# Performance work log

Hardware: AMD Instinct MI355X
Metric: run time of the kernel (lower is better)

The kernel has to match this reference:

```python
import jax, jax.numpy as jnp
import numpy as np

B, M, K, KNN = 2, 256, 64, 16
CXYZ, CFEAT = 3, 61
CIN = CXYZ + CFEAT  # 64
MLPS = [64, 128]
SUMM = sum(MLPS)    # 192
CALIB = 64
EXP = [256, 512]
OUT = 256
EPS = 1e-5


def bn(x, g, b):
    # BatchNorm eval mode with running_mean=0, running_var=1 (channel axis 1)
    shape = (1, -1) + (1,) * (x.ndim - 2)
    return x * (g / jnp.sqrt(1.0 + EPS)).reshape(shape) + b.reshape(shape)


def knn(x, k):
    xx = jnp.sum(x * x, axis=1)                      # (B, N)
    inner = jnp.einsum('bcn,bcm->bnm', x, x)         # (B, N, N)
    pd = 2.0 * inner - xx[:, :, None] - xx[:, None, :]
    return jax.lax.top_k(pd, k)[1]                   # (B, N, k)


def graph_feature(x, idx):
    # x: (B, C, N), idx: (B, N, k) -> (B, 2C, N, k)
    xt = jnp.transpose(x, (0, 2, 1))                 # (B, N, C)
    nb = jax.vmap(lambda a, i: a[i])(xt, idx)        # (B, N, k, C)
    ctr = xt[:, :, None, :]
    feat = jnp.concatenate([nb - ctr, jnp.broadcast_to(ctr, nb.shape)], axis=-1)
    return jnp.transpose(feat, (0, 3, 1, 2))


def forward(xyz, feats, e1_w, e1_g, e1_b, e2_w, e2_g, e2_b,
            cal1_w, cal1_g, cal1_b, cal2_w, cal2_bias,
            exp1_w, exp1_g, exp1_b, exp2_w, exp2_g, exp2_b,
            red_w, red_g, red_b, sc1_w, sc1_b, sc2_w, sc2_b,
            sc_n1_g, sc_n1_b, sc_n2_g, sc_n2_b):
    x3 = xyz.reshape(B * M, K, CXYZ).transpose(0, 2, 1)      # (BM, 3, K)
    f = feats.reshape(B * M, K, CFEAT).transpose(0, 2, 1)    # (BM, 61, K)
    idx = knn(x3, KNN)                                        # USE_FEATS_DIS=False: knn once on xyz
    x = jnp.concatenate([x3, f], axis=1)                      # (BM, 64, K)
    outs = []
    for W, g, b in ((e1_w, e1_g, e1_b), (e2_w, e2_g, e2_b)):
        gf = graph_feature(x, idx)                            # (BM, 2C, K, knn)
        y = jax.nn.relu(bn(jnp.einsum('oc,bcnk->bonk', W, gf), g, b))
        x = y.max(axis=-1)                                    # (BM, mlp_i, K)
        outs.append(x)
    x = jnp.concatenate(outs, axis=1)                         # (BM, 192, K)
    c = jax.nn.relu(bn(jnp.einsum('oc,bcn->bon', cal1_w, x), cal1_g, cal1_b))
    c = jnp.einsum('oc,bcn->bon', cal2_w, c) + cal2_bias[None, :, None]
    x = jax.nn.sigmoid(c) * x
    x = jax.nn.relu(bn(jnp.einsum('oc,bcn->bon', exp1_w, x), exp1_g, exp1_b))
    x = jax.nn.relu(bn(jnp.einsum('oc,bcn->bon', exp2_w, x), exp2_g, exp2_b))
    x = x.max(axis=-1).reshape(B, M, EXP[1]).transpose(0, 2, 1)  # (B, 512, M)
    x = jax.nn.relu(bn(jnp.einsum('oc,bcm->bom', red_w, x), red_g, red_b))
    x = bn(x + x, sc_n1_g, sc_n1_b)
    h = jax.nn.relu(jnp.einsum('oc,bcm->bom', sc1_w, x) + sc1_b[None, :, None])
    h = jnp.einsum('oc,bcm->bom', sc2_w, h) + sc2_b[None, :, None]
    x = bn(x + h, sc_n2_g, sc_n2_b)
    return x                                                  # (B, 256, M)


def setup_inputs() -> dict:
    key = jax.random.key(0)
    ks = jax.random.split(key, 16)
    w = lambda k, s: jax.random.normal(k, s, jnp.float32) * 0.05
    ones = lambda n: jnp.ones((n,), jnp.float32)
    zeros = lambda n: jnp.zeros((n,), jnp.float32)
    return {
        'xyz': jax.random.normal(ks[0], (B, M, K, CXYZ), jnp.float32),
        'feats': jax.random.normal(ks[1], (B, M, K, CFEAT), jnp.float32),
        'e1_w': w(ks[2], (MLPS[0], 2 * CIN)), 'e1_g': ones(MLPS[0]), 'e1_b': zeros(MLPS[0]),
        'e2_w': w(ks[3], (MLPS[1], 2 * MLPS[0])), 'e2_g': ones(MLPS[1]), 'e2_b': zeros(MLPS[1]),
        'cal1_w': w(ks[4], (CALIB, SUMM)), 'cal1_g': ones(CALIB), 'cal1_b': zeros(CALIB),
        'cal2_w': w(ks[5], (SUMM, CALIB)), 'cal2_bias': zeros(SUMM),
        'exp1_w': w(ks[6], (EXP[0], SUMM)), 'exp1_g': ones(EXP[0]), 'exp1_b': zeros(EXP[0]),
        'exp2_w': w(ks[7], (EXP[1], EXP[0])), 'exp2_g': ones(EXP[1]), 'exp2_b': zeros(EXP[1]),
        'red_w': w(ks[8], (OUT, EXP[1])), 'red_g': ones(OUT), 'red_b': zeros(OUT),
        'sc1_w': w(ks[9], (OUT, OUT)), 'sc1_b': zeros(OUT),
        'sc2_w': w(ks[10], (OUT, OUT)), 'sc2_b': zeros(OUT),
        'sc_n1_g': ones(OUT), 'sc_n1_b': zeros(OUT),
        'sc_n2_g': ones(OUT), 'sc_n2_b': zeros(OUT),
    }


def reference(xyz, feats, e1_w, e1_g, e1_b, e2_w, e2_g, e2_b,
              cal1_w, cal1_g, cal1_b, cal2_w, cal2_bias,
              exp1_w, exp1_g, exp1_b, exp2_w, exp2_g, exp2_b,
              red_w, red_g, red_b, sc1_w, sc1_b, sc2_w, sc2_b,
              sc_n1_g, sc_n1_b, sc_n2_g, sc_n2_b):
    return forward(xyz, feats, e1_w, e1_g, e1_b, e2_w, e2_g, e2_b,
                   cal1_w, cal1_g, cal1_b, cal2_w, cal2_bias,
                   exp1_w, exp1_g, exp1_b, exp2_w, exp2_g, exp2_b,
                   red_w, red_g, red_b, sc1_w, sc1_b, sc2_w, sc2_b,
                   sc_n1_g, sc_n1_b, sc_n2_g, sc_n2_b)
```

## Files before the change

### kernel.cpp

```cpp
#include <hip/hip_runtime.h>
#include <hip/hip_bf16.h>
#include <math.h>
#include <stddef.h>

#define DEV __device__ __forceinline__
__device__ const float BNS = 0.99999500003749968f;

typedef __bf16 bf16x8 __attribute__((ext_vector_type(8)));
typedef float  f32x4  __attribute__((ext_vector_type(4)));

DEV unsigned short f2bs(float v){
  union{ __hip_bfloat16 b; unsigned short u; } c; c.b=__float2bfloat16(v); return c.u;
}
DEV float bs2f(unsigned short u){
  union{ unsigned short u; __hip_bfloat16 b; } c; c.u=u; return __bfloat162float(c.b);
}


__global__ __launch_bounds__(256) void k_prep(const float* __restrict__ e1_w,
    const float* __restrict__ e2_w, const float* __restrict__ cal1_w,
    const float* __restrict__ cal2_w, const float* __restrict__ exp1_w,
    const float* __restrict__ exp2_w, unsigned short* __restrict__ Whi,
    unsigned short* __restrict__ Wlo,
    const float* __restrict__ red_w, const float* __restrict__ sc1_w,
    const float* __restrict__ sc2_w, float* __restrict__ Wt_red,
    float* __restrict__ Wt_s1, float* __restrict__ Wt_s2){
  __shared__ float s[32][33];
  int bid = blockIdx.x;
  if(bid < 896){
    const float* src; unsigned short *hi,*lo; int mode, O=0, i0;
    if(bid<32)      { src=e1_w;  hi=Whi;       lo=Wlo;       mode=1; O= 64; i0=bid*256; }
    else if(bid<96) { src=e2_w;  hi=Whi+8192;  lo=Wlo+8192;  mode=1; O=128; i0=(bid-32)*256; }
    else if(bid<144){ src=cal1_w;hi=Whi+24576; lo=Wlo+24576; mode=0;        i0=(bid-96)*256; }
    else if(bid<192){ src=cal2_w;hi=Whi+36864; lo=Wlo+36864; mode=0;        i0=(bid-144)*256; }
    else if(bid<384){ src=exp1_w;hi=Whi+49152; lo=Wlo+49152; mode=0;        i0=(bid-192)*256; }
    else            { src=exp2_w;hi=Whi+98304; lo=Wlo+98304; mode=0;        i0=(bid-384)*256; }
    int i = i0 + threadIdx.x;
    float v;
    if(mode==0) v = src[i];
    else {
      int row=i>>6, c=i&63;
      v = (row<O) ? src[row*128+c] : (src[(row-O)*128+64+c]-src[(row-O)*128+c]);
    }
    unsigned short h=f2bs(v); hi[i]=h; lo[i]=f2bs(v-bs2f(h));
  } else {
    int lb = bid-896;
    const float* in; float* out; int O,K;
    if(lb<128){ in=red_w; out=Wt_red; O=256; K=512; }
    else if(lb<192){ in=sc1_w; out=Wt_s1; O=256; K=256; lb-=128; }
    else { in=sc2_w; out=Wt_s2; O=256; K=256; lb-=192; }
    int nt=O>>5;
    int to=lb%nt, tk=lb/nt;
    int c=threadIdx.x&31, r8=threadIdx.x>>5;
    #pragma unroll
    for(int p=0;p<4;p++){
      int r=r8+p*8;
      s[r][c]=in[(size_t)(to*32+r)*K + tk*32 + c];
    }
    __syncthreads();
    #pragma unroll
    for(int p=0;p<4;p++){
      int r=r8+p*8;
      out[(size_t)(tk*32+r)*O + to*32 + c]=s[c][r];
    }
  }
}

__global__ __launch_bounds__(256) void k_knne12(const float* __restrict__ xyz,
    const float* __restrict__ feats,
    const unsigned short* __restrict__ W1h, const unsigned short* __restrict__ W1l,
    const unsigned short* __restrict__ W2h, const unsigned short* __restrict__ W2l,
    int* __restrict__ idxo, const float* __restrict__ g1, const float* __restrict__ b1,
    const float* __restrict__ g2, const float* __restrict__ b2,
    unsigned short* __restrict__ cat){
  __shared__ float bufA[64*65];
  __shared__ float bufB[64*65];
  __shared__ __align__(16) unsigned short sb[64*136];
  __shared__ int   ips[64*16];
  __shared__ float sx0[64], sx1[64], sx2[64], sxx[64];
  int bm = blockIdx.x;
  int tid = threadIdx.x, n = tid&63, s = tid>>6;
  int wid = tid>>6, lane = tid&63;
  int l15 = lane&15, q = lane>>4;
  if(s==0){
    const float* xp = xyz + (size_t)(bm*64+n)*3;
    float px=xp[0], py=xp[1], pz=xp[2];
    sx0[n]=px; sx1[n]=py; sx2[n]=pz; sxx[n]=px*px+py*py+pz*pz;
  }
  __syncthreads();
  {
    int p = lane>>2, seg = lane&3;
    int n1 = wid*16 + p;
    float px=sx0[n1], py=sx1[n1], pz=sx2[n1], xxn=sxx[n1];
    float pdr[16];
    #pragma unroll
    for(int t=0;t<16;t++){
      int m = seg*16+t;
      pdr[t] = 2.f*(px*sx0[m]+py*sx1[m]+pz*sx2[m]) - xxn - sxx[m];
    }
    for(int j=0;j<16;j++){
      float bv=-3.4e38f; int bi=seg*16;
      #pragma unroll
      for(int t=0;t<16;t++){ if(pdr[t]>bv){bv=pdr[t]; bi=seg*16+t;} }
      float ov=__shfl_xor(bv,1); int oi=__shfl_xor(bi,1);
      if(ov>bv || (ov==bv && oi<bi)){bv=ov;bi=oi;}
      ov=__shfl_xor(bv,2); oi=__shfl_xor(bi,2);
      if(ov>bv || (ov==bv && oi<bi)){bv=ov;bi=oi;}
      if(seg==0) ips[n1*16+j]=bi;
      if((bi>>4)==seg) pdr[bi&15]=-3.4e38f;
    }
  }
  {
    unsigned short* r = sb + n*136;
    if(s==0){
      float px=sx0[n], py=sx1[n], pz=sx2[n];
      unsigned short h;
      h=f2bs(px); r[0]=h; r[64]=f2bs(px-bs2f(h));
      h=f2bs(py); r[1]=h; r[65]=f2bs(py-bs2f(h));
      h=f2bs(pz); r[2]=h; r[66]=f2bs(pz-bs2f(h));
    }
    const float* fp = feats + (size_t)(bm*64+n)*61;
    #pragma unroll
    for(int t=0;t<16;t++){
      int cc = s*16+t;
      if(cc<61){
        float v=fp[cc]; unsigned short h=f2bs(v);
        r[3+cc]=h; r[64+3+cc]=f2bs(v-bs2f(h));
      }
    }
  }
  __syncthreads();
  #pragma unroll
  for(int t=0;t<4;t++) idxo[bm*1024 + tid*4 + t] = ips[tid*4 + t];
  {
    int rbase = ((wid<2)?0:64) + (wid&1)*32;
    f32x4 acc[2][4];
    #pragma unroll
    for(int a=0;a<2;a++)
      #pragma unroll
      for(int d=0;d<4;d++) acc[a][d]=(f32x4){0.f,0.f,0.f,0.f};
    #pragma unroll
    for(int kc=0;kc<2;kc++){
      int k0=kc*32;
      size_t a0=(size_t)(rbase+l15)*64 + k0 + q*8;
      size_t a1=(size_t)(rbase+16+l15)*64 + k0 + q*8;
      bf16x8 a0h=*(const bf16x8*)(W1h+a0), a0l=*(const bf16x8*)(W1l+a0);
      bf16x8 a1h=*(const bf16x8*)(W1h+a1), a1l=*(const bf16x8*)(W1l+a1);
      #pragma unroll
      for(int nt=0;nt<4;nt++){
        int row = nt*16 + l15;
        bf16x8 bh = *(const bf16x8*)&sb[row*136 + k0 + q*8];
        bf16x8 bl = *(const bf16x8*)&sb[row*136 + 64 + k0 + q*8];
        acc[0][nt]=__builtin_amdgcn_mfma_f32_16x16x32_bf16(a0h,bh,acc[0][nt],0,0,0);
        acc[0][nt]=__builtin_amdgcn_mfma_f32_16x16x32_bf16(a0h,bl,acc[0][nt],0,0,0);
        acc[0][nt]=__builtin_amdgcn_mfma_f32_16x16x32_bf16(a0l,bh,acc[0][nt],0,0,0);
        acc[1][nt]=__builtin_amdgcn_mfma_f32_16x16x32_bf16(a1h,bh,acc[1][nt],0,0,0);
        acc[1][nt]=__builtin_amdgcn_mfma_f32_16x16x32_bf16(a1h,bl,acc[1][nt],0,0,0);
        acc[1][nt]=__builtin_amdgcn_mfma_f32_16x16x32_bf16(a1l,bh,acc[1][nt],0,0,0);
      }
    }
    __syncthreads();
    float* dst = (wid<2)? bufA : bufB;
    int ro = (wid&1)*32;
    #pragma unroll
    for(int mt=0;mt<2;mt++)
      #pragma unroll
      for(int nt=0;nt<4;nt++)
        #pragma unroll
        for(int rr=0;rr<4;rr++)
          dst[(ro+mt*16+q*4+rr)*65 + nt*16+l15] = acc[mt][nt][rr];
  }
  __syncthreads();
  {
    int o = lane;
    float sc = g1[o]*BNS, bi = b1[o];
    #pragma unroll 4
    for(int j=0;j<16;j++){
      int nn = wid*16 + j;
      const int* ip = &ips[nn*16];
      float mz = -3.4e38f;
      #pragma unroll
      for(int k=0;k<16;k++) mz = fmaxf(mz, bufA[o*65 + ip[k]]);
      float v = fmaxf(sc*(mz + bufB[o*65 + nn]) + bi, 0.f);
      unsigned short hv = f2bs(v), lv = f2bs(v - bs2f(hv));
      size_t cb = ((size_t)bm*64+nn)*384 + o;
      cat[cb] = hv; cat[cb+192] = lv;
      sb[nn*136 + o] = hv; sb[nn*136 + 64 + o] = lv;
    }
  }
  for(int ch=0; ch<2; ch++){
    __syncthreads();
    int rbase = ((wid<2)?0:128) + ch*64 + (wid&1)*32;
    f32x4 acc[2][4];
    #pragma unroll
    for(int a=0;a<2;a++)
      #pragma unroll
      for(int d=0;d<4;d++) acc[a][d]=(f32x4){0.f,0.f,0.f,0.f};
    #pragma unroll
    for(int kc=0;kc<2;kc++){
      int k0=kc*32;
      size_t a0=(size_t)(rbase+l15)*64 + k0 + q*8;
      size_t a1=(size_t)(rbase+16+l15)*64 + k0 + q*8;
      bf16x8 a0h=*(const bf16x8*)(W2h+a0), a0l=*(const bf16x8*)(W2l+a0);
      bf16x8 a1h=*(const bf16x8*)(W2h+a1), a1l=*(const bf16x8*)(W2l+a1);
      #pragma unroll
      for(int nt=0;nt<4;nt++){
        int row = nt*16 + l15;
        bf16x8 bh = *(const bf16x8*)&sb[row*136 + k0 + q*8];
        bf16x8 bl = *(const bf16x8*)&sb[row*136 + 64 + k0 + q*8];
        acc[0][nt]=__builtin_amdgcn_mfma_f32_16x16x32_bf16(a0h,bh,acc[0][nt],0,0,0);
        acc[0][nt]=__builtin_amdgcn_mfma_f32_16x16x32_bf16(a0h,bl,acc[0][nt],0,0,0);
        acc[0][nt]=__builtin_amdgcn_mfma_f32_16x16x32_bf16(a0l,bh,acc[0][nt],0,0,0);
        acc[1][nt]=__builtin_amdgcn_mfma_f32_16x16x32_bf16(a1h,bh,acc[1][nt],0,0,0);
        acc[1][nt]=__builtin_amdgcn_mfma_f32_16x16x32_bf16(a1h,bl,acc[1][nt],0,0,0);
        acc[1][nt]=__builtin_amdgcn_mfma_f32_16x16x32_bf16(a1l,bh,acc[1][nt],0,0,0);
      }
    }
    __syncthreads();
    float* dst = (wid<2)? bufA : bufB;
    int ro = (wid&1)*32;
    #pragma unroll
    for(int mt=0;mt<2;mt++)
      #pragma unroll
      for(int nt=0;nt<4;nt++)
        #pragma unroll
        for(int rr=0;rr<4;rr++)
          dst[(ro+mt*16+q*4+rr)*65 + nt*16+l15] = acc[mt][nt][rr];
    __syncthreads();
    int o = ch*64 + lane;
    float sc = g2[o]*BNS, bi = b2[o];
    #pragma unroll 4
    for(int j=0;j<16;j++){
      int nn = wid*16 + j;
      const int* ip = &ips[nn*16];
      float mz = -3.4e38f;
      #pragma unroll
      for(int k=0;k<16;k++) mz = fmaxf(mz, bufA[lane*65 + ip[k]]);
      float v = fmaxf(sc*(mz + bufB[lane*65 + nn]) + bi, 0.f);
      unsigned short hv = f2bs(v);
      size_t cb = ((size_t)bm*64+nn)*384 + 64 + o;
      cat[cb] = hv; cat[cb+192] = f2bs(v - bs2f(hv));
    }
  }
}

__global__ __launch_bounds__(256) void k_cal(
    const unsigned short* __restrict__ Whi, const unsigned short* __restrict__ Wlo,
    unsigned short* __restrict__ cats,
    const float* __restrict__ c1g, const float* __restrict__ c1b,
    const float* __restrict__ c2bias){
  const unsigned short* c1w_h = Whi+24576; const unsigned short* c1w_l = Wlo+24576;
  const unsigned short* c2w_h = Whi+36864; const unsigned short* c2w_l = Wlo+36864;
  __shared__ __align__(16) unsigned short sW[64*64];
  __shared__ __align__(16) unsigned short sX[128*64];
  __shared__ __align__(16) unsigned short c1L[128*136];
  int rt = blockIdx.x;
  int tid = threadIdx.x, wid = tid>>6, lane = tid&63;
  int l15 = lane&15, q = lane>>4;
  f32x4 acc1[8];
  #pragma unroll
  for(int d=0;d<8;d++) acc1[d]=(f32x4){0.f,0.f,0.f,0.f};
  size_t xbase = (size_t)rt*128*384;
  for(int kc=0;kc<6;kc++){
    int k0=kc*32;
    __syncthreads();
    #pragma unroll
    for(int i=0;i<2;i++){
      int U = tid + i*256;
      int r = U>>3, up = U&7, u = up ^ (r&7);
      const unsigned short* src = (u<4)
        ? (c1w_h + (size_t)r*192 + k0 + u*8)
        : (c1w_l + (size_t)r*192 + k0 + (u-4)*8);
      *(uint4*)&sW[U*8] = *(const uint4*)src;
    }
    #pragma unroll
    for(int i=0;i<4;i++){
      int U = tid + i*256;
      int r = U>>3, up = U&7, u = up ^ (r&7);
      const unsigned short* src = cats + xbase + (size_t)r*384
        + (u<4 ? (size_t)(k0 + u*8) : (size_t)(192 + k0 + (u-4)*8));
      *(uint4*)&sX[U*8] = *(const uint4*)src;
    }
    __syncthreads();
    int o = wid*16 + l15;
    bf16x8 wh = *(const bf16x8*)&sW[(o*8 + ((  q) ^ (o&7)))*8];
    bf16x8 wl = *(const bf16x8*)&sW[(o*8 + ((4+q) ^ (o&7)))*8];
    #pragma unroll
    for(int nf=0;nf<8;nf++){
      int r = nf*16 + l15;
      bf16x8 xh = *(const bf16x8*)&sX[(r*8 + ((  q) ^ (r&7)))*8];
      bf16x8 xl = *(const bf16x8*)&sX[(r*8 + ((4+q) ^ (r&7)))*8];
      acc1[nf]=__builtin_amdgcn_mfma_f32_16x16x32_bf16(wh,xh,acc1[nf],0,0,0);
      acc1[nf]=__builtin_amdgcn_mfma_f32_16x16x32_bf16(wh,xl,acc1[nf],0,0,0);
      acc1[nf]=__builtin_amdgcn_mfma_f32_16x16x32_bf16(wl,xh,acc1[nf],0,0,0);
    }
  }
  {
    int ob0 = wid*16 + q*4;
    float s0[4], b0[4];
    #pragma unroll
    for(int r=0;r<4;r++){ s0[r]=c1g[ob0+r]*BNS; b0[r]=c1b[ob0+r]; }
    #pragma unroll
    for(int nf=0;nf<8;nf++){
      int n = nf*16 + l15;
      unsigned short hv[4], lv[4];
      #pragma unroll
      for(int r=0;r<4;r++){
        float v = fmaxf(acc1[nf][r]*s0[r]+b0[r], 0.f);
        hv[r]=f2bs(v); lv[r]=f2bs(v - bs2f(hv[r]));
      }
      *(ushort4*)&c1L[n*136 + ob0]      = make_ushort4(hv[0],hv[1],hv[2],hv[3]);
      *(ushort4*)&c1L[n*136 + 64 + ob0] = make_ushort4(lv[0],lv[1],lv[2],lv[3]);
    }
  }
  __syncthreads();
  f32x4 acc2[3][8];
  #pragma unroll
  for(int a=0;a<3;a++)
    #pragma unroll
    for(int d=0;d<8;d++) acc2[a][d]=(f32x4){0.f,0.f,0.f,0.f};
  #pragma unroll
  for(int kc=0;kc<2;kc++){
    int k0=kc*32;
    bf16x8 ah[3], al[3];
    #pragma unroll
    for(int mt=0;mt<3;mt++){
      int o = wid*48 + mt*16 + l15;
      ah[mt]=*(const bf16x8*)(c2w_h + (size_t)o*64 + k0 + q*8);
      al[mt]=*(const bf16x8*)(c2w_l + (size_t)o*64 + k0 + q*8);
    }
    #pragma unroll
    for(int nf=0;nf<8;nf++){
      int n = nf*16 + l15;
      bf16x8 bh = *(const bf16x8*)&c1L[n*136 + k0 + q*8];
      bf16x8 bl = *(const bf16x8*)&c1L[n*136 + 64 + k0 + q*8];
      #pragma unroll
      for(int mt=0;mt<3;mt++){
        acc2[mt][nf]=__builtin_amdgcn_mfma_f32_16x16x32_bf16(ah[mt],bh,acc2[mt][nf],0,0,0);
        acc2[mt][nf]=__builtin_amdgcn_mfma_f32_16x16x32_bf16(ah[mt],bl,acc2[mt][nf],0,0,0);
        acc2[mt][nf]=__builtin_amdgcn_mfma_f32_16x16x32_bf16(al[mt],bh,acc2[mt][nf],0,0,0);
      }
    }
  }
  #pragma unroll
  for(int mt=0;mt<3;mt++){
    int ob0 = wid*48 + mt*16 + q*4;
    float bi[4];
    #pragma unroll
    for(int r=0;r<4;r++) bi[r]=c2bias[ob0+r];
    #pragma unroll
    for(int nf=0;nf<8;nf++){
      size_t row = (size_t)rt*128 + nf*16 + l15;
      size_t rb = row*384;
      ushort4 hv = *(ushort4*)(cats + rb + ob0);
      ushort4 lv = *(ushort4*)(cats + rb + 192 + ob0);
      unsigned short h[4]={hv.x,hv.y,hv.z,hv.w}, l[4]={lv.x,lv.y,lv.z,lv.w};
      #pragma unroll
      for(int r=0;r<4;r++){
        float g = 1.f/(1.f+__expf(-(acc2[mt][nf][r]+bi[r])));
        float f = (bs2f(h[r])+bs2f(l[r]))*g;
        h[r]=f2bs(f); l[r]=f2bs(f-bs2f(h[r]));
      }
      *(ushort4*)(cats + rb + ob0)       = make_ushort4(h[0],h[1],h[2],h[3]);
      *(ushort4*)(cats + rb + 192 + ob0) = make_ushort4(l[0],l[1],l[2],l[3]);
    }
  }
}

template<int K, int BO, int EPI>
__global__ __launch_bounds__(256) void k_mm2(
    const unsigned short* __restrict__ Whi, const unsigned short* __restrict__ Wlo,
    const unsigned short* __restrict__ X, void* __restrict__ Og,
    const float* __restrict__ sg, const float* __restrict__ bg, int O){
  constexpr int WO = BO/4;
  constexpr int MT = WO/16;
  constexpr int WUNITS = BO*8;
  __shared__ __align__(16) unsigned short sW[BO*64];
  __shared__ __align__(16) unsigned short sX[128*64];
  int rt = blockIdx.x;
  int o0 = blockIdx.y*BO;
  int tid = threadIdx.x, wid = tid>>6, lane = tid&63;
  int l15 = lane&15, q = lane>>4;
  f32x4 acc[MT][8];
  #pragma unroll
  for(int a=0;a<MT;a++)
    #pragma unroll
    for(int d=0;d<8;d++) acc[a][d]=(f32x4){0.f,0.f,0.f,0.f};
  size_t xbase = (size_t)rt*128*2*K;
  for(int kc=0; kc<K/32; kc++){
    int k0 = kc*32;
    __syncthreads();
    #pragma unroll
    for(int i=0;i<WUNITS/256;i++){
      int U = tid + i*256;
      int r = U>>3, up = U&7, u = up ^ (r&7);
      const unsigned short* src = (u<4)
        ? (Whi + (size_t)(o0+r)*K + k0 + u*8)
        : (Wlo + (size_t)(o0+r)*K + k0 + (u-4)*8);
      *(uint4*)&sW[U*8] = *(const uint4*)src;
    }
    #pragma unroll
    for(int i=0;i<4;i++){
      int U = tid + i*256;
      int r = U>>3, up = U&7, u = up ^ (r&7);
      const unsigned short* src = X + xbase + (size_t)r*2*K
        + (u<4 ? (size_t)(k0 + u*8) : (size_t)(K + k0 + (u-4)*8));
      *(uint4*)&sX[U*8] = *(const uint4*)src;
    }
    __syncthreads();
    bf16x8 wf[MT][2];
    #pragma unroll
    for(int mt=0;mt<MT;mt++){
      int o = wid*WO + mt*16 + l15;
      wf[mt][0] = *(const bf16x8*)&sW[(o*8 + ((  q) ^ (o&7)))*8];
      wf[mt][1] = *(const bf16x8*)&sW[(o*8 + ((4+q) ^ (o&7)))*8];
    }
    #pragma unroll
    for(int nf=0;nf<8;nf++){
      int r = nf*16 + l15;
      bf16x8 xh = *(const bf16x8*)&sX[(r*8 + ((  q) ^ (r&7)))*8];
      bf16x8 xl = *(const bf16x8*)&sX[(r*8 + ((4+q) ^ (r&7)))*8];
      #pragma unroll
      for(int mt=0;mt<MT;mt++){
        acc[mt][nf]=__builtin_amdgcn_mfma_f32_16x16x32_bf16(wf[mt][0],xh,acc[mt][nf],0,0,0);
        acc[mt][nf]=__builtin_amdgcn_mfma_f32_16x16x32_bf16(wf[mt][0],xl,acc[mt][nf],0,0,0);
        acc[mt][nf]=__builtin_amdgcn_mfma_f32_16x16x32_bf16(wf[mt][1],xh,acc[mt][nf],0,0,0);
      }
    }
  }
  if(EPI==0){
    unsigned short* ob = (unsigned short*)Og;
    #pragma unroll
    for(int mt=0;mt<MT;mt++){
      int ob0 = o0 + wid*WO + mt*16 + q*4;
      float s0[4], b0[4];
      #pragma unroll
      for(int r=0;r<4;r++){ s0[r]=sg[ob0+r]*BNS; b0[r]=bg[ob0+r]; }
      #pragma unroll
      for(int nf=0;nf<8;nf++){
        size_t row = (size_t)rt*128 + nf*16 + l15;
        size_t rb = row*2*O;
        unsigned short hv[4], lv[4];
        #pragma unroll
        for(int r=0;r<4;r++){
          float v = fmaxf(acc[mt][nf][r]*s0[r]+b0[r], 0.f);
          hv[r]=f2bs(v); lv[r]=f2bs(v - bs2f(hv[r]));
        }
        *(ushort4*)(ob + rb + ob0)     = make_ushort4(hv[0],hv[1],hv[2],hv[3]);
        *(ushort4*)(ob + rb + O + ob0) = make_ushort4(lv[0],lv[1],lv[2],lv[3]);
      }
    }
  } else {
    float* pool = (float*)Og;
    #pragma unroll
    for(int mt=0;mt<MT;mt++){
      int ob0 = o0 + wid*WO + mt*16 + q*4;
      #pragma unroll
      for(int half=0;half<2;half++){
        int bm = 2*rt + half;
        int b = bm>>8, m = bm&255;
        #pragma unroll
        for(int r=0;r<4;r++){
          float s=sg[ob0+r]*BNS, bi=bg[ob0+r];
          float v = acc[mt][half*4+0][r]*s+bi;
          v = fmaxf(v, acc[mt][half*4+1][r]*s+bi);
          v = fmaxf(v, acc[mt][half*4+2][r]*s+bi);
          v = fmaxf(v, acc[mt][half*4+3][r]*s+bi);
          v = fmaxf(v, 0.f);
          v = fmaxf(v, __shfl_xor(v,1));
          v = fmaxf(v, __shfl_xor(v,2));
          v = fmaxf(v, __shfl_xor(v,4));
          v = fmaxf(v, __shfl_xor(v,8));
          if(l15==0) pool[((size_t)b*512 + ob0+r)*256 + m] = v;
        }
      }
    }
  }
}

__global__ __launch_bounds__(256) void k_headf(const float* __restrict__ Wt_red,
    const float* __restrict__ Wt_s1, const float* __restrict__ Wt_s2,
    const float* __restrict__ pool, float* __restrict__ Og,
    const float* __restrict__ red_g, const float* __restrict__ red_b,
    const float* __restrict__ n1g, const float* __restrict__ n1b,
    const float* __restrict__ s1b, const float* __restrict__ s2b,
    const float* __restrict__ n2g, const float* __restrict__ n2b){
  __shared__ float P[512*3];
  __shared__ float X1[256*3];
  __shared__ float H[256*3];
  int g = blockIdx.x;
  int b = g>>7, mg = g&127;
  int m0 = mg*2;
  int o = threadIdx.x;
  #pragma unroll
  for(int i=0;i<2;i++){
    int c = o + i*256;
    float2 v = *(const float2*)&pool[((size_t)b*512+c)*256 + m0];
    P[c*3+0]=v.x; P[c*3+1]=v.y;
  }
  __syncthreads();
  float a0,a1;
  a0=a1=0.f;
  #pragma unroll 8
  for(int c=0;c<512;c++){
    float w = Wt_red[c*256+o];
    a0 += w*P[c*3]; a1 += w*P[c*3+1];
  }
  float x0r,x1r;
  {
    float s=red_g[o]*BNS, bi=red_b[o], s1=n1g[o]*BNS, b1=n1b[o];
    float r0=fmaxf(a0*s+bi,0.f), r1=fmaxf(a1*s+bi,0.f);
    x0r=2.f*r0*s1+b1; x1r=2.f*r1*s1+b1;
    X1[o*3]=x0r; X1[o*3+1]=x1r;
  }
  __syncthreads();
  a0=a1=0.f;
  #pragma unroll 8
  for(int c=0;c<256;c++){
    float w = Wt_s1[c*256+o];
    a0 += w*X1[c*3]; a1 += w*X1[c*3+1];
  }
  {
    float bi=s1b[o];
    H[o*3]=fmaxf(a0+bi,0.f); H[o*3+1]=fmaxf(a1+bi,0.f);
  }
  __syncthreads();
  a0=a1=0.f;
  #pragma unroll 8
  for(int c=0;c<256;c++){
    float w = Wt_s2[c*256+o];
    a0 += w*H[c*3]; a1 += w*H[c*3+1];
  }
  {
    float bi=s2b[o], s2=n2g[o]*BNS, b2=n2b[o];
    float v0=(x0r+a0+bi)*s2+b2, v1=(x1r+a1+bi)*s2+b2;
    *(float2*)&Og[((size_t)b*256+o)*256 + m0] = make_float2(v0,v1);
  }
}

extern "C" void kernel_launch(void* const* d_in, const int* in_sizes, int n_in,
                              void* d_out, int out_size, void* d_ws, size_t ws_size,
                              hipStream_t stream){
  const float* xyz     =(const float*)d_in[0];
  const float* feats   =(const float*)d_in[1];
  const float* e1_w    =(const float*)d_in[2];
  const float* e1_g    =(const float*)d_in[3];
  const float* e1_b    =(const float*)d_in[4];
  const float* e2_w    =(const float*)d_in[5];
  const float* e2_g    =(const float*)d_in[6];
  const float* e2_b    =(const float*)d_in[7];
  const float* cal1_w  =(const float*)d_in[8];
  const float* cal1_g  =(const float*)d_in[9];
  const float* cal1_b  =(const float*)d_in[10];
  const float* cal2_w  =(const float*)d_in[11];
  const float* cal2_bias=(const float*)d_in[12];
  const float* exp1_w  =(const float*)d_in[13];
  const float* exp1_g  =(const float*)d_in[14];
  const float* exp1_b  =(const float*)d_in[15];
  const float* exp2_w  =(const float*)d_in[16];
  const float* exp2_g  =(const float*)d_in[17];
  const float* exp2_b  =(const float*)d_in[18];
  const float* red_w   =(const float*)d_in[19];
  const float* red_g   =(const float*)d_in[20];
  const float* red_b   =(const float*)d_in[21];
  const float* sc1_w   =(const float*)d_in[22];
  const float* sc1_b   =(const float*)d_in[23];
  const float* sc2_w   =(const float*)d_in[24];
  const float* sc2_b   =(const float*)d_in[25];
  const float* sc_n1_g =(const float*)d_in[26];
  const float* sc_n1_b =(const float*)d_in[27];
  const float* sc_n2_g =(const float*)d_in[28];
  const float* sc_n2_b =(const float*)d_in[29];

  char* wsb=(char*)d_ws;
  int*            idx =(int*)           (wsb);
  unsigned short* cats=(unsigned short*)(wsb + 10485760);
  unsigned short* p1s =(unsigned short*)(wsb + 35651584);
  float*          pool=(float*)         (wsb + 69206016);
  unsigned short* Whi =(unsigned short*)(wsb + 75497472);
  unsigned short* Wlo =(unsigned short*)(wsb + 76021760);
  float*          Wt_red=(float*)       (wsb + 76546048);
  float*          Wt_s1 =(float*)       (wsb + 77070336);
  float*          Wt_s2 =(float*)       (wsb + 77332480);
  unsigned short* e1e_h=Whi;          unsigned short* e1e_l=Wlo;
  unsigned short* e2e_h=Whi+8192;     unsigned short* e2e_l=Wlo+8192;
  unsigned short* e1w_h=Whi+49152;    unsigned short* e1w_l=Wlo+49152;
  unsigned short* e2w_h=Whi+98304;    unsigned short* e2w_l=Wlo+98304;

  k_prep      <<<1152,256,0,stream>>>(e1_w,e2_w,cal1_w,cal2_w,exp1_w,exp2_w,Whi,Wlo,
                                      red_w,sc1_w,sc2_w,Wt_red,Wt_s1,Wt_s2);
  k_knne12    <<<512,256,0,stream>>>(xyz,feats,e1e_h,e1e_l,e2e_h,e2e_l,idx,
                                     e1_g,e1_b,e2_g,e2_b,cats);
  k_cal       <<<256,256,0,stream>>>(Whi,Wlo,cats,cal1_g,cal1_b,cal2_bias);
  k_mm2<192,128,0><<<dim3(256,2),256,0,stream>>>(e1w_h,e1w_l,cats,(void*)p1s,exp1_g,exp1_b,256);
  k_mm2<256,128,2><<<dim3(256,4),256,0,stream>>>(e2w_h,e2w_l,p1s,(void*)pool,exp2_g,exp2_b,512);
  k_headf     <<<256,256,0,stream>>>(Wt_red,Wt_s1,Wt_s2,pool,(float*)d_out,
                                     red_g,red_b,sc_n1_g,sc_n1_b,sc1_b,sc2_b,sc_n2_g,sc_n2_b);
}
```

Measured before the change: 267.3 us.

## Fuse calibration and expansion MLPs into one per-group kernel, split head reduction

New measurement: 274.4 us. 1.03x slower.

```diff
diff --git a/kernel.cpp b/kernel.cpp
--- a/kernel.cpp
+++ b/kernel.cpp
@@ -9,11 +9,27 @@
 typedef __bf16 bf16x8 __attribute__((ext_vector_type(8)));
 typedef float  f32x4  __attribute__((ext_vector_type(4)));
 
+#define MF(a,b,c) __builtin_amdgcn_mfma_f32_16x16x32_bf16(a,b,c,0,0,0)
+
 DEV unsigned short f2bs(float v){
   union{ __hip_bfloat16 b; unsigned short u; } c; c.b=__float2bfloat16(v); return c.u;
 }
 DEV float bs2f(unsigned short u){
   union{ unsigned short u; __hip_bfloat16 b; } c; c.u=u; return __bfloat162float(c.b);
+}
+
+DEV void put_split(unsigned short* chunks, int n, int c, float v){
+  unsigned short hv=f2bs(v), lv=f2bs(v-bs2f(hv));
+  int cc=c>>5, u=(c>>3)&3, e=c&7;
+  unsigned short* base = chunks + cc*4096;
+  base[(n*8 + (u     ^ (n&7)))*8 + e] = hv;
+  base[(n*8 + ((u+4) ^ (n&7)))*8 + e] = lv;
+}
+DEV float get_split(const unsigned short* chunks, int n, int c){
+  int cc=c>>5, u=(c>>3)&3, e=c&7;
+  const unsigned short* base = chunks + cc*4096;
+  return bs2f(base[(n*8 + (u     ^ (n&7)))*8 + e])
+       + bs2f(base[(n*8 + ((u+4) ^ (n&7)))*8 + e]);
 }
 
 
@@ -70,7 +86,7 @@
     const float* __restrict__ feats,
     const unsigned short* __restrict__ W1h, const unsigned short* __restrict__ W1l,
     const unsigned short* __restrict__ W2h, const unsigned short* __restrict__ W2l,
-    int* __restrict__ idxo, const float* __restrict__ g1, const float* __restrict__ b1,
+    const float* __restrict__ g1, const float* __restrict__ b1,
     const float* __restrict__ g2, const float* __restrict__ b2,
     unsigned short* __restrict__ cat){
   __shared__ float bufA[64*65];
@@ -130,8 +146,6 @@
     }
   }
   __syncthreads();
-  #pragma unroll
-  for(int t=0;t<4;t++) idxo[bm*1024 + tid*4 + t] = ips[tid*4 + t];
   {
     int rbase = ((wid<2)?0:64) + (wid&1)*32;
     f32x4 acc[2][4];
@@ -151,12 +165,12 @@
         int row = nt*16 + l15;
         bf16x8 bh = *(const bf16x8*)&sb[row*136 + k0 + q*8];
         bf16x8 bl = *(const bf16x8*)&sb[row*136 + 64 + k0 + q*8];
-        acc[0][nt]=__builtin_amdgcn_mfma_f32_16x16x32_bf16(a0h,bh,acc[0][nt],0,0,0);
-        acc[0][nt]=__builtin_amdgcn_mfma_f32_16x16x32_bf16(a0h,bl,acc[0][nt],0,0,0);
-        acc[0][nt]=__builtin_amdgcn_mfma_f32_16x16x32_bf16(a0l,bh,acc[0][nt],0,0,0);
-        acc[1][nt]=__builtin_amdgcn_mfma_f32_16x16x32_bf16(a1h,bh,acc[1][nt],0,0,0);
-        acc[1][nt]=__builtin_amdgcn_mfma_f32_16x16x32_bf16(a1h,bl,acc[1][nt],0,0,0);
-        acc[1][nt]=__builtin_amdgcn_mfma_f32_16x16x32_bf16(a1l,bh,acc[1][nt],0,0,0);
+        acc[0][nt]=MF(a0h,bh,acc[0][nt]);
+        acc[0][nt]=MF(a0h,bl,acc[0][nt]);
+        acc[0][nt]=MF(a0l,bh,acc[0][nt]);
+        acc[1][nt]=MF(a1h,bh,acc[1][nt]);
+        acc[1][nt]=MF(a1h,bl,acc[1][nt]);
+        acc[1][nt]=MF(a1l,bh,acc[1][nt]);
       }
     }
     __syncthreads();
@@ -208,12 +222,12 @@
         int row = nt*16 + l15;
         bf16x8 bh = *(const bf16x8*)&sb[row*136 + k0 + q*8];
         bf16x8 bl = *(const bf16x8*)&sb[row*136 + 64 + k0 + q*8];
-        acc[0][nt]=__builtin_amdgcn_mfma_f32_16x16x32_bf16(a0h,bh,acc[0][nt],0,0,0);
-        acc[0][nt]=__builtin_amdgcn_mfma_f32_16x16x32_bf16(a0h,bl,acc[0][nt],0,0,0);
-        acc[0][nt]=__builtin_amdgcn_mfma_f32_16x16x32_bf16(a0l,bh,acc[0][nt],0,0,0);
-        acc[1][nt]=__builtin_amdgcn_mfma_f32_16x16x32_bf16(a1h,bh,acc[1][nt],0,0,0);
-        acc[1][nt]=__builtin_amdgcn_mfma_f32_16x16x32_bf16(a1h,bl,acc[1][nt],0,0,0);
-        acc[1][nt]=__builtin_amdgcn_mfma_f32_16x16x32_bf16(a1l,bh,acc[1][nt],0,0,0);
+        acc[0][nt]=MF(a0h,bh,acc[0][nt]);
+        acc[0][nt]=MF(a0h,bl,acc[0][nt]);
+        acc[0][nt]=MF(a0l,bh,acc[0][nt]);
+        acc[1][nt]=MF(a1h,bh,acc[1][nt]);
+        acc[1][nt]=MF(a1h,bl,acc[1][nt]);
+        acc[1][nt]=MF(a1l,bh,acc[1][nt]);
       }
     }
     __syncthreads();
@@ -244,241 +258,188 @@
   }
 }
 
-__global__ __launch_bounds__(256) void k_cal(
+__global__ __launch_bounds__(512) void k_mlp(
     const unsigned short* __restrict__ Whi, const unsigned short* __restrict__ Wlo,
-    unsigned short* __restrict__ cats,
+    const unsigned short* __restrict__ cats,
     const float* __restrict__ c1g, const float* __restrict__ c1b,
-    const float* __restrict__ c2bias){
-  const unsigned short* c1w_h = Whi+24576; const unsigned short* c1w_l = Wlo+24576;
-  const unsigned short* c2w_h = Whi+36864; const unsigned short* c2w_l = Wlo+36864;
-  __shared__ __align__(16) unsigned short sW[64*64];
-  __shared__ __align__(16) unsigned short sX[128*64];
-  __shared__ __align__(16) unsigned short c1L[128*136];
-  int rt = blockIdx.x;
+    const float* __restrict__ c2bias,
+    const float* __restrict__ e1g, const float* __restrict__ e1b,
+    const float* __restrict__ e2g, const float* __restrict__ e2b,
+    float* __restrict__ pool){
+  __shared__ __align__(16) unsigned short sXc[6*4096];
+  __shared__ __align__(16) unsigned short R1[8*4096];
+  int bm = blockIdx.x;
   int tid = threadIdx.x, wid = tid>>6, lane = tid&63;
   int l15 = lane&15, q = lane>>4;
-  f32x4 acc1[8];
+  size_t xb = (size_t)bm*24576;
   #pragma unroll
-  for(int d=0;d<8;d++) acc1[d]=(f32x4){0.f,0.f,0.f,0.f};
-  size_t xbase = (size_t)rt*128*384;
-  for(int kc=0;kc<6;kc++){
-    int k0=kc*32;
-    __syncthreads();
-    #pragma unroll
-    for(int i=0;i<2;i++){
-      int U = tid + i*256;
-      int r = U>>3, up = U&7, u = up ^ (r&7);
-      const unsigned short* src = (u<4)
-        ? (c1w_h + (size_t)r*192 + k0 + u*8)
-        : (c1w_l + (size_t)r*192 + k0 + (u-4)*8);
-      *(uint4*)&sW[U*8] = *(const uint4*)src;
-    }
-    #pragma unroll
-    for(int i=0;i<4;i++){
-      int U = tid + i*256;
-      int r = U>>3, up = U&7, u = up ^ (r&7);
-      const unsigned short* src = cats + xbase + (size_t)r*384
-        + (u<4 ? (size_t)(k0 + u*8) : (size_t)(192 + k0 + (u-4)*8));
-      *(uint4*)&sX[U*8] = *(const uint4*)src;
-    }
-    __syncthreads();
-    int o = wid*16 + l15;
-    bf16x8 wh = *(const bf16x8*)&sW[(o*8 + ((  q) ^ (o&7)))*8];
-    bf16x8 wl = *(const bf16x8*)&sW[(o*8 + ((4+q) ^ (o&7)))*8];
-    #pragma unroll
-    for(int nf=0;nf<8;nf++){
-      int r = nf*16 + l15;
-      bf16x8 xh = *(const bf16x8*)&sX[(r*8 + ((  q) ^ (r&7)))*8];
-      bf16x8 xl = *(const bf16x8*)&sX[(r*8 + ((4+q) ^ (r&7)))*8];
-      acc1[nf]=__builtin_amdgcn_mfma_f32_16x16x32_bf16(wh,xh,acc1[nf],0,0,0);
-      acc1[nf]=__builtin_amdgcn_mfma_f32_16x16x32_bf16(wh,xl,acc1[nf],0,0,0);
-      acc1[nf]=__builtin_amdgcn_mfma_f32_16x16x32_bf16(wl,xh,acc1[nf],0,0,0);
-    }
-  }
-  {
-    int ob0 = wid*16 + q*4;
-    float s0[4], b0[4];
-    #pragma unroll
-    for(int r=0;r<4;r++){ s0[r]=c1g[ob0+r]*BNS; b0[r]=c1b[ob0+r]; }
-    #pragma unroll
-    for(int nf=0;nf<8;nf++){
-      int n = nf*16 + l15;
-      unsigned short hv[4], lv[4];
-      #pragma unroll
-      for(int r=0;r<4;r++){
-        float v = fmaxf(acc1[nf][r]*s0[r]+b0[r], 0.f);
-        hv[r]=f2bs(v); lv[r]=f2bs(v - bs2f(hv[r]));
-      }
-      *(ushort4*)&c1L[n*136 + ob0]      = make_ushort4(hv[0],hv[1],hv[2],hv[3]);
-      *(ushort4*)&c1L[n*136 + 64 + ob0] = make_ushort4(lv[0],lv[1],lv[2],lv[3]);
-    }
-  }
-  __syncthreads();
-  f32x4 acc2[3][8];
-  #pragma unroll
-  for(int a=0;a<3;a++)
-    #pragma unroll
-    for(int d=0;d<8;d++) acc2[a][d]=(f32x4){0.f,0.f,0.f,0.f};
-  #pragma unroll
-  for(int kc=0;kc<2;kc++){
-    int k0=kc*32;
-    bf16x8 ah[3], al[3];
-    #pragma unroll
-    for(int mt=0;mt<3;mt++){
-      int o = wid*48 + mt*16 + l15;
-      ah[mt]=*(const bf16x8*)(c2w_h + (size_t)o*64 + k0 + q*8);
-      al[mt]=*(const bf16x8*)(c2w_l + (size_t)o*64 + k0 + q*8);
-    }
-    #pragma unroll
-    for(int nf=0;nf<8;nf++){
-      int n = nf*16 + l15;
-      bf16x8 bh = *(const bf16x8*)&c1L[n*136 + k0 + q*8];
-      bf16x8 bl = *(const bf16x8*)&c1L[n*136 + 64 + k0 + q*8];
-      #pragma unroll
-      for(int mt=0;mt<3;mt++){
-        acc2[mt][nf]=__builtin_amdgcn_mfma_f32_16x16x32_bf16(ah[mt],bh,acc2[mt][nf],0,0,0);
-        acc2[mt][nf]=__builtin_amdgcn_mfma_f32_16x16x32_bf16(ah[mt],bl,acc2[mt][nf],0,0,0);
-        acc2[mt][nf]=__builtin_amdgcn_mfma_f32_16x16x32_bf16(al[mt],bh,acc2[mt][nf],0,0,0);
-      }
-    }
-  }
-  #pragma unroll
-  for(int mt=0;mt<3;mt++){
-    int ob0 = wid*48 + mt*16 + q*4;
-    float bi[4];
-    #pragma unroll
-    for(int r=0;r<4;r++) bi[r]=c2bias[ob0+r];
-    #pragma unroll
-    for(int nf=0;nf<8;nf++){
-      size_t row = (size_t)rt*128 + nf*16 + l15;
-      size_t rb = row*384;
-      ushort4 hv = *(ushort4*)(cats + rb + ob0);
-      ushort4 lv = *(ushort4*)(cats + rb + 192 + ob0);
-      unsigned short h[4]={hv.x,hv.y,hv.z,hv.w}, l[4]={lv.x,lv.y,lv.z,lv.w};
-      #pragma unroll
-      for(int r=0;r<4;r++){
-        float g = 1.f/(1.f+__expf(-(acc2[mt][nf][r]+bi[r])));
-        float f = (bs2f(h[r])+bs2f(l[r]))*g;
-        h[r]=f2bs(f); l[r]=f2bs(f-bs2f(h[r]));
-      }
-      *(ushort4*)(cats + rb + ob0)       = make_ushort4(h[0],h[1],h[2],h[3]);
-      *(ushort4*)(cats + rb + 192 + ob0) = make_ushort4(l[0],l[1],l[2],l[3]);
-    }
-  }
-}
-
-template<int K, int BO, int EPI>
-__global__ __launch_bounds__(256) void k_mm2(
-    const unsigned short* __restrict__ Whi, const unsigned short* __restrict__ Wlo,
-    const unsigned short* __restrict__ X, void* __restrict__ Og,
-    const float* __restrict__ sg, const float* __restrict__ bg, int O){
-  constexpr int WO = BO/4;
-  constexpr int MT = WO/16;
-  constexpr int WUNITS = BO*8;
-  __shared__ __align__(16) unsigned short sW[BO*64];
-  __shared__ __align__(16) unsigned short sX[128*64];
-  int rt = blockIdx.x;
-  int o0 = blockIdx.y*BO;
-  int tid = threadIdx.x, wid = tid>>6, lane = tid&63;
-  int l15 = lane&15, q = lane>>4;
-  f32x4 acc[MT][8];
-  #pragma unroll
-  for(int a=0;a<MT;a++)
-    #pragma unroll
-    for(int d=0;d<8;d++) acc[a][d]=(f32x4){0.f,0.f,0.f,0.f};
-  size_t xbase = (size_t)rt*128*2*K;
-  for(int kc=0; kc<K/32; kc++){
-    int k0 = kc*32;
-    __syncthreads();
-    #pragma unroll
-    for(int i=0;i<WUNITS/256;i++){
-      int U = tid + i*256;
-      int r = U>>3, up = U&7, u = up ^ (r&7);
-      const unsigned short* src = (u<4)
-        ? (Whi + (size_t)(o0+r)*K + k0 + u*8)
-        : (Wlo + (size_t)(o0+r)*K + k0 + (u-4)*8);
-      *(uint4*)&sW[U*8] = *(const uint4*)src;
-    }
-    #pragma unroll
-    for(int i=0;i<4;i++){
-      int U = tid + i*256;
-      int r = U>>3, up = U&7, u = up ^ (r&7);
-      const unsigned short* src = X + xbase + (size_t)r*2*K
-        + (u<4 ? (size_t)(k0 + u*8) : (size_t)(K + k0 + (u-4)*8));
-      *(uint4*)&sX[U*8] = *(const uint4*)src;
-    }
-    __syncthreads();
-    bf16x8 wf[MT][2];
-    #pragma unroll
-    for(int mt=0;mt<MT;mt++){
-      int o = wid*WO + mt*16 + l15;
-      wf[mt][0] = *(const bf16x8*)&sW[(o*8 + ((  q) ^ (o&7)))*8];
-      wf[mt][1] = *(const bf16x8*)&sW[(o*8 + ((4+q) ^ (o&7)))*8];
-    }
-    #pragma unroll
-    for(int nf=0;nf<8;nf++){
-      int r = nf*16 + l15;
-      bf16x8 xh = *(const bf16x8*)&sX[(r*8 + ((  q) ^ (r&7)))*8];
-      bf16x8 xl = *(const bf16x8*)&sX[(r*8 + ((4+q) ^ (r&7)))*8];
-      #pragma unroll
-      for(int mt=0;mt<MT;mt++){
-        acc[mt][nf]=__builtin_amdgcn_mfma_f32_16x16x32_bf16(wf[mt][0],xh,acc[mt][nf],0,0,0);
-        acc[mt][nf]=__builtin_amdgcn_mfma_f32_16x16x32_bf16(wf[mt][0],xl,acc[mt][nf],0,0,0);
-        acc[mt][nf]=__builtin_amdgcn_mfma_f32_16x16x32_bf16(wf[mt][1],xh,acc[mt][nf],0,0,0);
-      }
-    }
-  }
-  if(EPI==0){
-    unsigned short* ob = (unsigned short*)Og;
-    #pragma unroll
-    for(int mt=0;mt<MT;mt++){
-      int ob0 = o0 + wid*WO + mt*16 + q*4;
-      float s0[4], b0[4];
-      #pragma unroll
-      for(int r=0;r<4;r++){ s0[r]=sg[ob0+r]*BNS; b0[r]=bg[ob0+r]; }
-      #pragma unroll
-      for(int nf=0;nf<8;nf++){
-        size_t row = (size_t)rt*128 + nf*16 + l15;
-        size_t rb = row*2*O;
-        unsigned short hv[4], lv[4];
+  for(int i=0;i<6;i++){
+    int U = tid + i*512;
+    int kc = U>>9, w = U&511, rr = w>>3, up = w&7, u = up ^ (rr&7);
+    const unsigned short* src = cats + xb + (size_t)rr*384
+      + (u<4 ? (kc*32 + u*8) : (192 + kc*32 + (u-4)*8));
+    *(uint4*)&sXc[kc*4096 + w*8] = *(const uint4*)src;
+  }
+  __syncthreads();
+  {
+    int ot = wid>>1, rh = wid&1;
+    f32x4 a0={0.f,0.f,0.f,0.f}, a1={0.f,0.f,0.f,0.f};
+    const unsigned short* wh = Whi + 24576;
+    const unsigned short* wl = Wlo + 24576;
+    #pragma unroll
+    for(int kc=0;kc<6;kc++){
+      size_t wo = (size_t)(ot*16+l15)*192 + kc*32 + q*8;
+      bf16x8 ah=*(const bf16x8*)(wh+wo), al=*(const bf16x8*)(wl+wo);
+      const unsigned short* cb = sXc + kc*4096;
+      int r0 = rh*32+l15, r1 = rh*32+16+l15;
+      bf16x8 xh0=*(const bf16x8*)&cb[(r0*8+((  q)^(r0&7)))*8];
+      bf16x8 xl0=*(const bf16x8*)&cb[(r0*8+((4+q)^(r0&7)))*8];
+      bf16x8 xh1=*(const bf16x8*)&cb[(r1*8+((  q)^(r1&7)))*8];
+      bf16x8 xl1=*(const bf16x8*)&cb[(r1*8+((4+q)^(r1&7)))*8];
+      a0=MF(ah,xh0,a0); a1=MF(ah,xh1,a1);
+      a0=MF(ah,xl0,a0); a1=MF(ah,xl1,a1);
+      a0=MF(al,xh0,a0); a1=MF(al,xh1,a1);
+    }
+    float s[4], bb[4];
+    #pragma unroll
+    for(int rr=0;rr<4;rr++){ int c=ot*16+q*4+rr; s[rr]=c1g[c]*BNS; bb[rr]=c1b[c]; }
+    #pragma unroll
+    for(int rr=0;rr<4;rr++){
+      int c=ot*16+q*4+rr;
+      put_split(R1, rh*32+l15,    c, fmaxf(a0[rr]*s[rr]+bb[rr],0.f));
+      put_split(R1, rh*32+16+l15, c, fmaxf(a1[rr]*s[rr]+bb[rr],0.f));
+    }
+  }
+  __syncthreads();
+  {
+    f32x4 ac[6];
+    #pragma unroll
+    for(int i=0;i<6;i++) ac[i]=(f32x4){0.f,0.f,0.f,0.f};
+    const unsigned short* wh = Whi + 36864;
+    const unsigned short* wl = Wlo + 36864;
+    #pragma unroll
+    for(int kc=0;kc<2;kc++){
+      const unsigned short* cb = R1 + kc*4096;
+      #pragma unroll
+      for(int i=0;i<6;i++){
+        int j = wid*6+i, ot=j>>2, nf=j&3;
+        size_t wo=(size_t)(ot*16+l15)*64 + kc*32 + q*8;
+        bf16x8 ah=*(const bf16x8*)(wh+wo), al=*(const bf16x8*)(wl+wo);
+        int r=nf*16+l15;
+        bf16x8 xh=*(const bf16x8*)&cb[(r*8+((  q)^(r&7)))*8];
+        bf16x8 xl=*(const bf16x8*)&cb[(r*8+((4+q)^(r&7)))*8];
+        ac[i]=MF(ah,xh,ac[i]); ac[i]=MF(ah,xl,ac[i]); ac[i]=MF(al,xh,ac[i]);
+      }
+    }
+    #pragma unroll
+    for(int i=0;i<6;i++){
+      int j=wid*6+i, ot=j>>2, nf=j&3, n=nf*16+l15;
+      #pragma unroll
+      for(int rr=0;rr<4;rr++){
+        int c=ot*16+q*4+rr;
+        float gv = 1.f/(1.f+__expf(-(ac[i][rr]+c2bias[c])));
+        put_split(sXc, n, c, get_split(sXc,n,c)*gv);
+      }
+    }
+  }
+  __syncthreads();
+  {
+    f32x4 ac[2][4];
+    #pragma unroll
+    for(int a=0;a<2;a++)
+      #pragma unroll
+      for(int d=0;d<4;d++) ac[a][d]=(f32x4){0.f,0.f,0.f,0.f};
+    const unsigned short* wh=Whi+49152; const unsigned short* wl=Wlo+49152;
+    int ob = wid*32;
+    #pragma unroll
+    for(int kc=0;kc<6;kc++){
+      bf16x8 ah[2], al[2];
+      #pragma unroll
+      for(int mt=0;mt<2;mt++){
+        size_t wo=(size_t)(ob+mt*16+l15)*192 + kc*32 + q*8;
+        ah[mt]=*(const bf16x8*)(wh+wo); al[mt]=*(const bf16x8*)(wl+wo);
+      }
+      const unsigned short* cb = sXc + kc*4096;
+      #pragma unroll
+      for(int nf=0;nf<4;nf++){
+        int r=nf*16+l15;
+        bf16x8 xh=*(const bf16x8*)&cb[(r*8+((  q)^(r&7)))*8];
+        bf16x8 xl=*(const bf16x8*)&cb[(r*8+((4+q)^(r&7)))*8];
+        ac[0][nf]=MF(ah[0],xh,ac[0][nf]); ac[1][nf]=MF(ah[1],xh,ac[1][nf]);
+        ac[0][nf]=MF(ah[0],xl,ac[0][nf]); ac[1][nf]=MF(ah[1],xl,ac[1][nf]);
+        ac[0][nf]=MF(al[0],xh,ac[0][nf]); ac[1][nf]=MF(al[1],xh,ac[1][nf]);
+      }
+    }
+    #pragma unroll
+    for(int mt=0;mt<2;mt++){
+      float s[4], bb[4];
+      #pragma unroll
+      for(int rr=0;rr<4;rr++){ int c=ob+mt*16+q*4+rr; s[rr]=e1g[c]*BNS; bb[rr]=e1b[c]; }
+      #pragma unroll
+      for(int nf=0;nf<4;nf++){
+        int n=nf*16+l15;
         #pragma unroll
-        for(int r=0;r<4;r++){
-          float v = fmaxf(acc[mt][nf][r]*s0[r]+b0[r], 0.f);
-          hv[r]=f2bs(v); lv[r]=f2bs(v - bs2f(hv[r]));
+        for(int rr=0;rr<4;rr++){
+          int c=ob+mt*16+q*4+rr;
+          put_split(R1, n, c, fmaxf(ac[mt][nf][rr]*s[rr]+bb[rr],0.f));
         }
-        *(ushort4*)(ob + rb + ob0)     = make_ushort4(hv[0],hv[1],hv[2],hv[3]);
-        *(ushort4*)(ob + rb + O + ob0) = make_ushort4(lv[0],lv[1],lv[2],lv[3]);
-      }
-    }
-  } else {
-    float* pool = (float*)Og;
-    #pragma unroll
-    for(int mt=0;mt<MT;mt++){
-      int ob0 = o0 + wid*WO + mt*16 + q*4;
-      #pragma unroll
-      for(int half=0;half<2;half++){
-        int bm = 2*rt + half;
-        int b = bm>>8, m = bm&255;
+      }
+    }
+  }
+  __syncthreads();
+  {
+    f32x4 ac[4][4];
+    #pragma unroll
+    for(int a=0;a<4;a++)
+      #pragma unroll
+      for(int d=0;d<4;d++) ac[a][d]=(f32x4){0.f,0.f,0.f,0.f};
+    const unsigned short* wh=Whi+98304; const unsigned short* wl=Wlo+98304;
+    int ob = wid*64;
+    for(int kc=0;kc<8;kc++){
+      bf16x8 ah[4], al[4];
+      #pragma unroll
+      for(int mt=0;mt<4;mt++){
+        size_t wo=(size_t)(ob+mt*16+l15)*256 + kc*32 + q*8;
+        ah[mt]=*(const bf16x8*)(wh+wo); al[mt]=*(const bf16x8*)(wl+wo);
+      }
+      const unsigned short* cb = R1 + kc*4096;
+      #pragma unroll
+      for(int nf=0;nf<4;nf++){
+        int r=nf*16+l15;
+        bf16x8 xh=*(const bf16x8*)&cb[(r*8+((  q)^(r&7)))*8];
+        bf16x8 xl=*(const bf16x8*)&cb[(r*8+((4+q)^(r&7)))*8];
         #pragma unroll
-        for(int r=0;r<4;r++){
-          float s=sg[ob0+r]*BNS, bi=bg[ob0+r];
-          float v = acc[mt][half*4+0][r]*s+bi;
-          v = fmaxf(v, acc[mt][half*4+1][r]*s+bi);
-          v = fmaxf(v, acc[mt][half*4+2][r]*s+bi);
-          v = fmaxf(v, acc[mt][half*4+3][r]*s+bi);
-          v = fmaxf(v, 0.f);
-          v = fmaxf(v, __shfl_xor(v,1));
-          v = fmaxf(v, __shfl_xor(v,2));
-          v = fmaxf(v, __shfl_xor(v,4));
-          v = fmaxf(v, __shfl_xor(v,8));
-          if(l15==0) pool[((size_t)b*512 + ob0+r)*256 + m] = v;
-        }
-      }
-    }
-  }
-}
-
-__global__ __launch_bounds__(256) void k_headf(const float* __restrict__ Wt_red,
+        for(int mt=0;mt<4;mt++) ac[mt][nf]=MF(ah[mt],xh,ac[mt][nf]);
+        #pragma unroll
+        for(int mt=0;mt<4;mt++) ac[mt][nf]=MF(ah[mt],xl,ac[mt][nf]);
+        #pragma unroll
+        for(int mt=0;mt<4;mt++) ac[mt][nf]=MF(al[mt],xh,ac[mt][nf]);
+      }
+    }
+    int b = bm>>8, m = bm&255;
+    #pragma unroll
+    for(int mt=0;mt<4;mt++){
+      float s[4], bb[4];
+      #pragma unroll
+      for(int rr=0;rr<4;rr++){ int c=ob+mt*16+q*4+rr; s[rr]=e2g[c]*BNS; bb[rr]=e2b[c]; }
+      #pragma unroll
+      for(int rr=0;rr<4;rr++){
+        float v = ac[mt][0][rr]*s[rr]+bb[rr];
+        v = fmaxf(v, ac[mt][1][rr]*s[rr]+bb[rr]);
+        v = fmaxf(v, ac[mt][2][rr]*s[rr]+bb[rr]);
+        v = fmaxf(v, ac[mt][3][rr]*s[rr]+bb[rr]);
+        v = fmaxf(v, 0.f);
+        v = fmaxf(v, __shfl_xor(v,1));
+        v = fmaxf(v, __shfl_xor(v,2));
+        v = fmaxf(v, __shfl_xor(v,4));
+        v = fmaxf(v, __shfl_xor(v,8));
+        if(l15==0) pool[((size_t)b*512 + ob+mt*16+q*4+rr)*256 + m] = v;
+      }
+    }
+  }
+}
+
+__global__ __launch_bounds__(512) void k_headf(const float* __restrict__ Wt_red,
     const float* __restrict__ Wt_s1, const float* __restrict__ Wt_s2,
     const float* __restrict__ pool, float* __restrict__ Og,
     const float* __restrict__ red_g, const float* __restrict__ red_b,
@@ -488,50 +449,71 @@
   __shared__ float P[512*3];
   __shared__ float X1[256*3];
   __shared__ float H[256*3];
+  __shared__ float PB[256*5];
   int g = blockIdx.x;
   int b = g>>7, mg = g&127;
   int m0 = mg*2;
-  int o = threadIdx.x;
-  #pragma unroll
-  for(int i=0;i<2;i++){
-    int c = o + i*256;
+  int tid = threadIdx.x;
+  int o = tid&255, h = tid>>8;
+  {
+    int c = tid;
     float2 v = *(const float2*)&pool[((size_t)b*512+c)*256 + m0];
     P[c*3+0]=v.x; P[c*3+1]=v.y;
   }
   __syncthreads();
-  float a0,a1;
-  a0=a1=0.f;
-  #pragma unroll 8
-  for(int c=0;c<512;c++){
-    float w = Wt_red[c*256+o];
-    a0 += w*P[c*3]; a1 += w*P[c*3+1];
-  }
+  float a0=0.f, a1=0.f;
+  {
+    int c0 = h*256;
+    #pragma unroll 8
+    for(int i=0;i<256;i++){
+      int c = c0+i;
+      float w = Wt_red[c*256+o];
+      a0 += w*P[c*3]; a1 += w*P[c*3+1];
+    }
+  }
+  PB[o*5+h*2]=a0; PB[o*5+h*2+1]=a1;
+  __syncthreads();
+  a0 = PB[o*5]+PB[o*5+2]; a1 = PB[o*5+1]+PB[o*5+3];
   float x0r,x1r;
   {
     float s=red_g[o]*BNS, bi=red_b[o], s1=n1g[o]*BNS, b1=n1b[o];
     float r0=fmaxf(a0*s+bi,0.f), r1=fmaxf(a1*s+bi,0.f);
     x0r=2.f*r0*s1+b1; x1r=2.f*r1*s1+b1;
-    X1[o*3]=x0r; X1[o*3+1]=x1r;
-  }
-  __syncthreads();
-  a0=a1=0.f;
-  #pragma unroll 8
-  for(int c=0;c<256;c++){
-    float w = Wt_s1[c*256+o];
-    a0 += w*X1[c*3]; a1 += w*X1[c*3+1];
-  }
+    if(h==0){ X1[o*3]=x0r; X1[o*3+1]=x1r; }
+  }
+  __syncthreads();
+  a0=0.f; a1=0.f;
+  {
+    int c0 = h*128;
+    #pragma unroll 8
+    for(int i=0;i<128;i++){
+      int c = c0+i;
+      float w = Wt_s1[c*256+o];
+      a0 += w*X1[c*3]; a1 += w*X1[c*3+1];
+    }
+  }
+  PB[o*5+h*2]=a0; PB[o*5+h*2+1]=a1;
+  __syncthreads();
+  a0 = PB[o*5]+PB[o*5+2]; a1 = PB[o*5+1]+PB[o*5+3];
   {
     float bi=s1b[o];
-    H[o*3]=fmaxf(a0+bi,0.f); H[o*3+1]=fmaxf(a1+bi,0.f);
-  }
-  __syncthreads();
-  a0=a1=0.f;
-  #pragma unroll 8
-  for(int c=0;c<256;c++){
-    float w = Wt_s2[c*256+o];
-    a0 += w*H[c*3]; a1 += w*H[c*3+1];
-  }
-  {
+    if(h==0){ H[o*3]=fmaxf(a0+bi,0.f); H[o*3+1]=fmaxf(a1+bi,0.f); }
+  }
+  __syncthreads();
+  a0=0.f; a1=0.f;
+  {
+    int c0 = h*128;
+    #pragma unroll 8
+    for(int i=0;i<128;i++){
+      int c = c0+i;
+      float w = Wt_s2[c*256+o];
+      a0 += w*H[c*3]; a1 += w*H[c*3+1];
+    }
+  }
+  PB[o*5+h*2]=a0; PB[o*5+h*2+1]=a1;
+  __syncthreads();
+  if(h==0){
+    a0 = PB[o*5]+PB[o*5+2]; a1 = PB[o*5+1]+PB[o*5+3];
     float bi=s2b[o], s2=n2g[o]*BNS, b2=n2b[o];
     float v0=(x0r+a0+bi)*s2+b2, v1=(x1r+a1+bi)*s2+b2;
     *(float2*)&Og[((size_t)b*256+o)*256 + m0] = make_float2(v0,v1);
@@ -573,9 +555,7 @@
   const float* sc_n2_b =(const float*)d_in[29];
 
   char* wsb=(char*)d_ws;
-  int*            idx =(int*)           (wsb);
   unsigned short* cats=(unsigned short*)(wsb + 10485760);
-  unsigned short* p1s =(unsigned short*)(wsb + 35651584);
   float*          pool=(float*)         (wsb + 69206016);
   unsigned short* Whi =(unsigned short*)(wsb + 75497472);
   unsigned short* Wlo =(unsigned short*)(wsb + 76021760);
@@ -584,16 +564,13 @@
   float*          Wt_s2 =(float*)       (wsb + 77332480);
   unsigned short* e1e_h=Whi;          unsigned short* e1e_l=Wlo;
   unsigned short* e2e_h=Whi+8192;     unsigned short* e2e_l=Wlo+8192;
-  unsigned short* e1w_h=Whi+49152;    unsigned short* e1w_l=Wlo+49152;
-  unsigned short* e2w_h=Whi+98304;    unsigned short* e2w_l=Wlo+98304;
 
   k_prep      <<<1152,256,0,stream>>>(e1_w,e2_w,cal1_w,cal2_w,exp1_w,exp2_w,Whi,Wlo,
                                       red_w,sc1_w,sc2_w,Wt_red,Wt_s1,Wt_s2);
-  k_knne12    <<<512,256,0,stream>>>(xyz,feats,e1e_h,e1e_l,e2e_h,e2e_l,idx,
+  k_knne12    <<<512,256,0,stream>>>(xyz,feats,e1e_h,e1e_l,e2e_h,e2e_l,
                                      e1_g,e1_b,e2_g,e2_b,cats);
-  k_cal       <<<256,256,0,stream>>>(Whi,Wlo,cats,cal1_g,cal1_b,cal2_bias);
-  k_mm2<192,128,0><<<dim3(256,2),256,0,stream>>>(e1w_h,e1w_l,cats,(void*)p1s,exp1_g,exp1_b,256);
-  k_mm2<256,128,2><<<dim3(256,4),256,0,stream>>>(e2w_h,e2w_l,p1s,(void*)pool,exp2_g,exp2_b,512);
-  k_headf     <<<256,256,0,stream>>>(Wt_red,Wt_s1,Wt_s2,pool,(float*)d_out,
+  k_mlp       <<<512,512,0,stream>>>(Whi,Wlo,cats,cal1_g,cal1_b,cal2_bias,
+                                     exp1_g,exp1_b,exp2_g,exp2_b,pool);
+  k_headf     <<<256,512,0,stream>>>(Wt_red,Wt_s1,Wt_s2,pool,(float*)d_out,
                                      red_g,red_b,sc_n1_g,sc_n1_b,sc1_b,sc2_b,sc_n2_g,sc_n2_b);
 }
```
